# Optimization experiments

Hardware: AMD Instinct MI355X
Metric: run time of the kernel (lower is better)

Reference implementation:

```python
import jax, jax.numpy as jnp
import numpy as np

NUM_HEADS = 8
DIM = 384
KSIZE = 9  # res_kernel_size


def _moe_fc(x2d, gate_w, gate_b, w0, b0, w1, b1):
    # NaiveGate with top_k=1: softmax over a single top-1 logit == 1.0, so the
    # SparseDispatcher dispatch/exp/mul/log combine reduces exactly to selecting
    # the argmax expert's output per token.
    logits = x2d @ gate_w + gate_b                      # [T, 2]
    sel = jnp.argmax(logits, axis=-1)[:, None]          # [T, 1]
    y0 = x2d @ w0.T + b0
    y1 = x2d @ w1.T + b1
    return jnp.where(sel == 0, y0, y1)


def _forward(x, qkv_gate_w, qkv_gate_b, qkv_w0, qkv_w1,
             proj_gate_w, proj_gate_b, proj_w0, proj_b0, proj_w1, proj_b1,
             dconv_w):
    B, N, C = x.shape
    h, hd = NUM_HEADS, C // NUM_HEADS
    xt = x.reshape(-1, C)
    zero3 = jnp.zeros((3 * C,), x.dtype)  # qkv_bias=False
    qkv = _moe_fc(xt, qkv_gate_w, qkv_gate_b, qkv_w0, zero3, qkv_w1, zero3)
    qkv = qkv.reshape(B, N, 3, h, hd).transpose(2, 0, 3, 1, 4)  # [3,B,h,N,d]
    q, k, v = qkv[0], qkv[1], qkv[2]

    q = q / jnp.linalg.norm(q, axis=-1, keepdims=True)
    k = k / jnp.linalg.norm(k, axis=-1, keepdims=True)
    scale1 = jnp.mean(jnp.abs(q))
    scale2 = jnp.mean(jnp.abs(k))
    # straight-through binarization: fwd value = (x>0)*scale, grad flows via clamp(x,0,1)
    cq = jnp.clip(q, 0.0, 1.0)
    q = jax.lax.stop_gradient((q > 0).astype(q.dtype) * scale1 - cq) + cq
    ck = jnp.clip(k, 0.0, 1.0)
    k = jax.lax.stop_gradient((k > 0).astype(k.dtype) * scale2 - ck) + ck

    # depthwise residual conv over the token axis: v is [B, h, N, d], kernel (9,1)
    dconv_v = jax.lax.conv_general_dilated(
        v, dconv_w, window_strides=(1, 1), padding=[(KSIZE // 2, KSIZE // 2), (0, 0)],
        feature_group_count=h, dimension_numbers=("NCHW", "OIHW", "NCHW"))

    # linear-attention reorder: (K^T V) first -> O(N d^2)
    attn = jnp.einsum("bhnd,bhne->bhde", k, v)          # [B,h,d,d]
    out = 0.5 * v - (1.0 / jnp.pi) * jnp.einsum("bhnd,bhde->bhne", q, attn)
    out = out / jnp.linalg.norm(out, axis=-1, keepdims=True)
    out = out + dconv_v
    out = out.transpose(0, 2, 1, 3).reshape(B, N, C)

    out = _moe_fc(out.reshape(-1, C), proj_gate_w, proj_gate_b,
                  proj_w0, proj_b0, proj_w1, proj_b1)
    return out.reshape(B, N, C)


def setup_inputs() -> dict:
    key = jax.random.key(0)
    ks = jax.random.split(key, 12)
    B, N, C = 8, 4096, DIM
    s = 0.02
    return {
        "x": jax.random.normal(ks[0], (B, N, C), jnp.float32),
        "H": 64,
        "W": 64,
        "qkv_gate_w": jax.random.normal(ks[1], (C, 2), jnp.float32) * s,
        "qkv_gate_b": jnp.zeros((2,), jnp.float32),
        "qkv_w0": jax.random.normal(ks[2], (3 * C, C), jnp.float32) * s,
        "qkv_w1": jax.random.normal(ks[3], (3 * C, C), jnp.float32) * s,
        "proj_gate_w": jax.random.normal(ks[4], (C, 2), jnp.float32) * s,
        "proj_gate_b": jnp.zeros((2,), jnp.float32),
        "proj_w0": jax.random.normal(ks[5], (C, C), jnp.float32) * s,
        "proj_b0": jnp.zeros((C,), jnp.float32),
        "proj_w1": jax.random.normal(ks[6], (C, C), jnp.float32) * s,
        "proj_b1": jnp.zeros((C,), jnp.float32),
        "dconv_w": jax.random.normal(ks[7], (NUM_HEADS, 1, KSIZE, 1), jnp.float32) * s,
    }


def reference(x, H, W, qkv_gate_w, qkv_gate_b, qkv_w0, qkv_w1,
              proj_gate_w, proj_gate_b, proj_w0, proj_b0, proj_w1, proj_b1,
              dconv_w):
    # H, W are unused by the math (kept for signature fidelity)
    return _forward(x, qkv_gate_w, qkv_gate_b, qkv_w0, qkv_w1,
                    proj_gate_w, proj_gate_b, proj_w0, proj_b0, proj_w1, proj_b1,
                    dconv_w)
```

## Files before the change

kernel.cpp:

```cpp
#include <hip/hip_runtime.h>
#include <hip/hip_bf16.h>

#define BB 8
#define NN 4096
#define CC 384
#define HH 8
#define DD 48
#define TT (BB*NN)
#define CAP (TT + 128)
#define NQ ((size_t)BB*HH*NN*DD)
#define LISTCAP 32768

static_assert(CAP % 128 == 0, "cap");

typedef __attribute__((ext_vector_type(8))) short bf16x8;
typedef __attribute__((ext_vector_type(4))) float f32x4;

__device__ __forceinline__ float waveRedSum(float v){
  #pragma unroll
  for (int o = 32; o > 0; o >>= 1) v += __shfl_xor(v, o);
  return v;
}

__device__ __forceinline__ unsigned short f2bf(float f){
  unsigned u = __float_as_uint(f);
  u += 0x7FFFu + ((u >> 16) & 1u);
  return (unsigned short)(u >> 16);
}
__device__ __forceinline__ float bf2f(unsigned short h){
  return __uint_as_float(((unsigned)h) << 16);
}

__global__ void k_init(int* __restrict__ perm0, int* __restrict__ perm1, int* __restrict__ cur){
  int i = blockIdx.x * 256 + threadIdx.x;
  if (i < 8) cur[i] = 0;
  if (i < CAP){ perm0[i] = -1; perm1[i] = -1; }
}

__global__ void k_cvt_split(const float* __restrict__ src, unsigned short* __restrict__ hi,
                            unsigned short* __restrict__ lo, int n4){
  int i = blockIdx.x*256 + threadIdx.x;
  if (i >= n4) return;
  float4 v = ((const float4*)src)[i];
  float f[4] = {v.x, v.y, v.z, v.w};
  unsigned short h[4], l[4];
  #pragma unroll
  for (int j = 0; j < 4; j++){
    h[j] = f2bf(f[j]);
    l[j] = f2bf(f[j] - bf2f(h[j]));
  }
  uint2 hv, lv;
  hv.x = h[0] | ((unsigned)h[1] << 16); hv.y = h[2] | ((unsigned)h[3] << 16);
  lv.x = l[0] | ((unsigned)l[1] << 16); lv.y = l[2] | ((unsigned)l[3] << 16);
  ((uint2*)hi)[i] = hv;
  ((uint2*)lo)[i] = lv;
}

__global__ void k_gate_scatter(const float* __restrict__ X,
                               const float* __restrict__ gw, const float* __restrict__ gb,
                               int* __restrict__ perm, int* __restrict__ cur,
                               unsigned char* __restrict__ selb){
  const int lane = threadIdx.x & 63;
  const int wave = threadIdx.x >> 6;
  float gd[6];
  #pragma unroll
  for (int j = 0; j < 6; j++){
    int c = lane + 64*j;
    gd[j] = gw[c*2+1] - gw[c*2];
  }
  const float gbd = gb[1] - gb[0];
  const int tok0 = (blockIdx.x*4 + wave) * 32;
  unsigned mask = 0u;
  for (int i = 0; i < 32; i++){
    const float* xr = X + (size_t)(tok0 + i) * CC;
    float d = 0.f;
    #pragma unroll
    for (int j = 0; j < 6; j++) d = fmaf(xr[lane + 64*j], gd[j], d);
    d = waveRedSum(d);
    if (d + gbd > 0.f) mask |= (1u << i);
  }
  int n1 = __popc(mask), n0 = 32 - n1;
  int b0 = 0, b1 = 0;
  if (lane == 0){
    b0 = atomicAdd(cur + 0, n0);
    b1 = atomicAdd(cur + 1, n1);
  }
  b0 = __shfl(b0, 0); b1 = __shfl(b1, 0);
  if (lane < 32){
    int sel = (mask >> lane) & 1;
    unsigned below = mask & ((1u << lane) - 1u);
    int r1 = __popc(below);
    int r0 = lane - r1;
    int idx = sel ? (CAP - 1 - (b1 + r1)) : (b0 + r0);
    perm[idx] = tok0 + lane;
    selb[tok0 + lane] = (unsigned char)sel;
  }
}

__global__ void k_gate2(const float* __restrict__ gpart, const float* __restrict__ gb,
                        int* __restrict__ perm, int* __restrict__ cur){
  const int t = blockIdx.x*256 + threadIdx.x;
  const int lane = threadIdx.x & 63;
  const float gbd = gb[1] - gb[0];
  float4 a = ((const float4*)(gpart + (size_t)t*8))[0];
  float4 c = ((const float4*)(gpart + (size_t)t*8))[1];
  float d = ((a.x + a.y) + (a.z + a.w)) + ((c.x + c.y) + (c.z + c.w)) + gbd;
  bool sel = d > 0.f;
  unsigned long long m = __ballot(sel);
  int n1 = (int)__popcll(m);
  int b0 = 0, b1 = 0;
  if (lane == 0){
    b0 = atomicAdd(cur + 0, 64 - n1);
    b1 = atomicAdd(cur + 1, n1);
  }
  b0 = __shfl(b0, 0); b1 = __shfl(b1, 0);
  unsigned long long below = m & ((1ull << lane) - 1ull);
  int r1 = (int)__popcll(below);
  int r0 = lane - r1;
  int idx = sel ? (CAP - 1 - (b1 + r1)) : (b0 + r0);
  perm[idx] = t;
}

template<int NCOLS, int PASSES, bool IS_QKV>
__global__ __launch_bounds__(256, 2)
void k_gemm_mfma(const unsigned short* __restrict__ Ahi_g, const unsigned short* __restrict__ Alo_g,
                 const unsigned short* __restrict__ W0h, const unsigned short* __restrict__ W0l,
                 const unsigned short* __restrict__ W1h, const unsigned short* __restrict__ W1l,
                 const float* __restrict__ bias0, const float* __restrict__ bias1,
                 const int* __restrict__ perm, const int* __restrict__ cur,
                 unsigned short* __restrict__ oq, unsigned short* __restrict__ ok,
                 float* __restrict__ ov, float* __restrict__ oproj,
                 int* __restrict__ tlist, int* __restrict__ tcnt)
{
  constexpr int GDX = NCOLS / 128;
  constexpr int NWG = GDX * (CAP/128);
  constexpr int NB = (PASSES == 3) ? 2 : 1;
  __shared__ unsigned short As[NB][128*32];
  __shared__ unsigned short Bs[NB][128*32];
  __shared__ int permv[128];

  int orig = blockIdx.y * GDX + blockIdx.x;
  constexpr int qq = NWG >> 3, rr = NWG & 7;
  int xcd = orig & 7, slot = orig >> 3;
  int logical = (xcd < rr) ? (xcd*(qq+1) + slot) : (rr*(qq+1) + (xcd-rr)*qq + slot);
  const int bx = logical % GDX, by = logical / GDX;

  const int tid = threadIdx.x;
  const int m0 = by * 128, n0 = bx * 128;
  if (tid < 128) permv[tid] = perm[m0 + tid];
  __syncthreads();
  const int expert = (m0 > cur[0]) ? 1 : 0;
  const unsigned short* Wh = expert ? W1h : W0h;
  const unsigned short* Wl = expert ? W1l : W0l;

  const int c0 = tid, c1 = tid + 256;
  const int r0 = c0 >> 2, r1 = c1 >> 2;
  const int s0 = (((c0 & 3) ^ ((r0 >> 1) & 3))) * 8;
  const int s1 = (((c1 & 3) ^ ((r1 >> 1) & 3))) * 8;
  int t0 = permv[r0]; if (t0 < 0) t0 = 0;
  int t1 = permv[r1]; if (t1 < 0) t1 = 0;
  const unsigned short* a0h = Ahi_g + (size_t)t0*CC + s0;
  const unsigned short* a1h = Ahi_g + (size_t)t1*CC + s1;
  const unsigned short* b0h = Wh + (size_t)(n0 + r0)*CC + s0;
  const unsigned short* b1h = Wh + (size_t)(n0 + r1)*CC + s1;
  const unsigned short* a0l = nullptr; const unsigned short* a1l = nullptr;
  const unsigned short* b0l = nullptr; const unsigned short* b1l = nullptr;
  if constexpr (PASSES == 3){
    a0l = Alo_g + (size_t)t0*CC + s0;
    a1l = Alo_g + (size_t)t1*CC + s1;
    b0l = Wl + (size_t)(n0 + r0)*CC + s0;
    b1l = Wl + (size_t)(n0 + r1)*CC + s1;
  }
  const int d0 = c0*8, d1 = c1*8;

  const int lane = tid & 63;
  const int wv = tid >> 6, wr = wv >> 1, wc2 = wv & 1;
  const int lr = lane & 15, lg = lane >> 4;

  f32x4 acc[4][4];
  #pragma unroll
  for (int i = 0; i < 4; i++)
    #pragma unroll
    for (int j = 0; j < 4; j++) acc[i][j] = (f32x4){0.f, 0.f, 0.f, 0.f};

  int aoff[4], boff[4];
  #pragma unroll
  for (int f = 0; f < 4; f++){
    int ra = wr*64 + f*16 + lr;
    aoff[f] = ra*32 + ((lg ^ ((ra >> 1) & 3)) * 8);
    int rb = wc2*64 + f*16 + lr;
    boff[f] = rb*32 + ((lg ^ ((rb >> 1) & 3)) * 8);
  }

  #define GLD(gp, lp) __builtin_amdgcn_global_load_lds( \
      (const __attribute__((address_space(1))) void*)(gp), \
      (__attribute__((address_space(3))) void*)(lp), 16, 0, 0)

  for (int ko = 0; ko < CC; ko += 32){
    GLD(a0h + ko, &As[0][d0]);
    GLD(a1h + ko, &As[0][d1]);
    GLD(b0h + ko, &Bs[0][d0]);
    GLD(b1h + ko, &Bs[0][d1]);
    if constexpr (PASSES == 3){
      GLD(a0l + ko, &As[1][d0]);
      GLD(a1l + ko, &As[1][d1]);
      GLD(b0l + ko, &Bs[1][d0]);
      GLD(b1l + ko, &Bs[1][d1]);
    }
    __syncthreads();
    bf16x8 ah[4], bh[4], al[4], bl[4];
    #pragma unroll
    for (int f = 0; f < 4; f++){
      ah[f] = *(const bf16x8*)&As[0][aoff[f]];
      bh[f] = *(const bf16x8*)&Bs[0][boff[f]];
      if constexpr (PASSES == 3){
        al[f] = *(const bf16x8*)&As[1][aoff[f]];
        bl[f] = *(const bf16x8*)&Bs[1][boff[f]];
      }
    }
    #pragma unroll
    for (int mf = 0; mf < 4; mf++)
      #pragma unroll
      for (int nf = 0; nf < 4; nf++){
        acc[mf][nf] = __builtin_amdgcn_mfma_f32_16x16x32_bf16(ah[mf], bh[nf], acc[mf][nf], 0, 0, 0);
        if constexpr (PASSES == 3){
          acc[mf][nf] = __builtin_amdgcn_mfma_f32_16x16x32_bf16(al[mf], bh[nf], acc[mf][nf], 0, 0, 0);
          acc[mf][nf] = __builtin_amdgcn_mfma_f32_16x16x32_bf16(ah[mf], bl[nf], acc[mf][nf], 0, 0, 0);
        }
      }
    __syncthreads();
  }
  #undef GLD

  #pragma unroll
  for (int mf = 0; mf < 4; mf++){
    #pragma unroll
    for (int j = 0; j < 4; j++){
      const int rl = wr*64 + mf*16 + lg*4 + j;
      const int t = permv[rl];
      if (t < 0) continue;
      const int b = t >> 12, nn = t & 4095;
      #pragma unroll
      for (int nf = 0; nf < 4; nf++){
        const int col = n0 + wc2*64 + nf*16 + lr;
        const float val = acc[mf][nf][j];
        if constexpr (IS_QKV){
          const int which = col / CC;
          const int rem = col - which*CC;
          const int h = rem / DD;
          const int e = rem - h*DD;
          const size_t off = (((size_t)b*HH + h)*NN + nn)*DD + e;
          if (which == 0){
            oq[off] = f2bf(val);
            if (fabsf(val) < 2.5e-5f){
              int pq = atomicAdd(tcnt, 1);
              if (pq < LISTCAP) tlist[pq] = (int)off;
            }
          } else if (which == 1){
            ok[off] = f2bf(val);
            if (fabsf(val) < 2.5e-5f){
              int pq = atomicAdd(tcnt, 1);
              if (pq < LISTCAP) tlist[pq] = (int)(off + NQ);
            }
          } else {
            ov[off] = val;
          }
        } else {
          const float* bs = expert ? bias1 : bias0;
          oproj[(size_t)t*CC + col] = val + bs[col];
        }
      }
    }
  }
}

__global__ void k_topup_fix(unsigned short* __restrict__ qb, unsigned short* __restrict__ kb,
                            const int* __restrict__ list, const int* __restrict__ cnt,
                            const float* __restrict__ x,
                            const float* __restrict__ w0, const float* __restrict__ w1,
                            const unsigned char* __restrict__ selb){
  const int lane = threadIdx.x & 63;
  const int gw = (blockIdx.x*256 + threadIdx.x) >> 6;
  const int nwaves = gridDim.x * 4;
  int n = cnt[0]; if (n > LISTCAP) n = LISTCAP;
  for (int e = gw; e < n; e += nwaves){
    int idx = list[e];
    int isK = (idx >= (int)NQ);
    int li = isK ? idx - (int)NQ : idx;
    int d = li % DD; int rest = li / DD;
    int nn = rest & 4095; int bh = rest >> 12;
    int b = bh >> 3, h = bh & 7;
    int t = b*NN + nn;
    int col = (isK ? CC : 0) + h*DD + d;
    const float* w = selb[t] ? w1 : w0;
    const float* xr = x + (size_t)t*CC;
    const float* wr = w + (size_t)col*CC;
    float s = 0.f;
    #pragma unroll
    for (int j = 0; j < 6; j++) s = fmaf(xr[lane + 64*j], wr[lane + 64*j], s);
    s = waveRedSum(s);
    if (lane == 0) (isK ? kb : qb)[li] = f2bf(s);
  }
}

__global__ void k_scales(const unsigned short* __restrict__ qb, const unsigned short* __restrict__ kb,
                         float* __restrict__ part){
  __shared__ float sq[256], sk[256];
  const int row = blockIdx.x*256 + threadIdx.x;
  const uint4* qp = (const uint4*)(qb + (size_t)row*DD);
  const uint4* kp = (const uint4*)(kb + (size_t)row*DD);
  float qss = 0.f, qsa = 0.f, kss = 0.f, ksa = 0.f;
  #pragma unroll
  for (int j = 0; j < 6; j++){
    uint4 u = qp[j];
    unsigned w[4] = {u.x, u.y, u.z, u.w};
    #pragma unroll
    for (int q2 = 0; q2 < 4; q2++){
      float f0 = bf2f((unsigned short)(w[q2] & 0xFFFFu));
      float f1 = bf2f((unsigned short)(w[q2] >> 16));
      qss = fmaf(f0, f0, qss); qsa += fabsf(f0);
      qss = fmaf(f1, f1, qss); qsa += fabsf(f1);
    }
    uint4 v = kp[j];
    unsigned w2[4] = {v.x, v.y, v.z, v.w};
    #pragma unroll
    for (int q2 = 0; q2 < 4; q2++){
      float f0 = bf2f((unsigned short)(w2[q2] & 0xFFFFu));
      float f1 = bf2f((unsigned short)(w2[q2] >> 16));
      kss = fmaf(f0, f0, kss); ksa += fabsf(f0);
      kss = fmaf(f1, f1, kss); ksa += fabsf(f1);
    }
  }
  sq[threadIdx.x] = qsa / sqrtf(qss);
  sk[threadIdx.x] = ksa / sqrtf(kss);
  __syncthreads();
  for (int s = 128; s > 0; s >>= 1){
    if (threadIdx.x < s){ sq[threadIdx.x] += sq[threadIdx.x+s]; sk[threadIdx.x] += sk[threadIdx.x+s]; }
    __syncthreads();
  }
  if (threadIdx.x == 0){
    part[blockIdx.x*2+0] = sq[0];
    part[blockIdx.x*2+1] = sk[0];
  }
}

__global__ void k_scales_reduce(const float* __restrict__ part, float* __restrict__ scalesb){
  __shared__ float sq[256], sk[256];
  const int t = threadIdx.x;
  float aq = 0.f, ak = 0.f;
  for (int i = t; i < 1024; i += 256){ aq += part[2*i]; ak += part[2*i+1]; }
  sq[t] = aq; sk[t] = ak;
  __syncthreads();
  for (int s = 128; s > 0; s >>= 1){
    if (t < s){ sq[t] += sq[t+s]; sk[t] += sk[t+s]; }
    __syncthreads();
  }
  if (t == 0){
    scalesb[0] = sq[0] * (1.0f/12582912.0f);
    scalesb[1] = sk[0] * (1.0f/12582912.0f);
  }
}

__global__ void k_attn_partial(const unsigned short* __restrict__ kb, const float* __restrict__ vb,
                               float* __restrict__ part){
  __shared__ float ks[64][48];
  __shared__ float vs[64][48];
  const int bh = blockIdx.x, seg = blockIdx.y;
  const int tid = threadIdx.x;
  const int ti = tid >> 5;
  const int tj = (tid >> 2) & 7;
  const int sl = tid & 3;
  const int dd0 = ti*6, ee0 = tj*6;
  const unsigned short* kbase = kb + ((size_t)bh*NN + seg*512) * DD;
  const float* vbase = vb + ((size_t)bh*NN + seg*512) * DD;
  float acc[6][6] = {};
  for (int c = 0; c < 8; c++){
    __syncthreads();
    for (int f = tid*2; f < 3072; f += 512){
      unsigned kk2 = *(const unsigned*)(kbase + c*3072 + f);
      float2 vv2 = *(const float2*)(vbase + c*3072 + f);
      (&ks[0][0])[f]   = ((short)(unsigned short)(kk2 & 0xFFFFu) > 0) ? 1.f : 0.f;
      (&ks[0][0])[f+1] = ((short)(unsigned short)(kk2 >> 16) > 0) ? 1.f : 0.f;
      (&vs[0][0])[f]   = vv2.x;
      (&vs[0][0])[f+1] = vv2.y;
    }
    __syncthreads();
    for (int nl = sl*16; nl < sl*16 + 16; nl++){
      float kk[6], vv[6];
      #pragma unroll
      for (int i = 0; i < 6; i++){ kk[i] = ks[nl][dd0+i]; vv[i] = vs[nl][ee0+i]; }
      #pragma unroll
      for (int i = 0; i < 6; i++)
        #pragma unroll
        for (int j = 0; j < 6; j++)
          acc[i][j] = fmaf(kk[i], vv[j], acc[i][j]);
    }
  }
  float* p = part + ((size_t)seg*64 + bh) * (DD*DD);
  #pragma unroll
  for (int i = 0; i < 6; i++)
    #pragma unroll
    for (int j = 0; j < 6; j++){
      float a = acc[i][j];
      a += __shfl_xor(a, 1);
      a += __shfl_xor(a, 2);
      if (sl == 0) p[(dd0+i)*48 + (ee0+j)] = a;
    }
}

__global__ void k_attn_reduce(const float* __restrict__ part, const float* __restrict__ scalesb,
                              unsigned short* __restrict__ aTh, unsigned short* __restrict__ aTl){
  const int bh = blockIdx.x;
  const float s2 = scalesb[1];
  for (int f = threadIdx.x; f < 3072; f += 256){
    const int e = f >> 6, d = f & 63;
    float s = 0.f;
    if (d < 48){
      #pragma unroll
      for (int seg = 0; seg < 8; seg++) s += part[((size_t)seg*64 + bh)*2304 + d*48 + e];
      s *= s2;
    }
    unsigned short hi = f2bf(s);
    aTh[(size_t)bh*3072 + f] = hi;
    aTl[(size_t)bh*3072 + f] = f2bf(s - bf2f(hi));
  }
}

__global__ __launch_bounds__(256, 4)
void k_fused(const unsigned short* __restrict__ qb, const float* __restrict__ vb,
             const unsigned short* __restrict__ aTh, const unsigned short* __restrict__ aTl,
             const float* __restrict__ scalesb, const float* __restrict__ dw,
             const float* __restrict__ pgw,
             unsigned short* __restrict__ intermh, float* __restrict__ gpart){
  __shared__ unsigned short aT[2][48*72];
  __shared__ float S_lds[128*48];
  __shared__ float wc[16];
  const int chunk = blockIdx.x;
  const int bh = blockIdx.y;
  const int b = bh >> 3, h = bh & 7;
  const int tid = threadIdx.x;
  const int lane = tid & 63, w = tid >> 6;
  const int lr = lane & 15, lg = lane >> 4;

  for (int idx = tid; idx < 384; idx += 256){
    const int e = idx >> 3, sl = idx & 7;
    *(uint4*)&aT[0][e*72 + sl*8] = *(const uint4*)(aTh + (size_t)bh*3072 + e*64 + sl*8);
    *(uint4*)&aT[1][e*72 + sl*8] = *(const uint4*)(aTl + (size_t)bh*3072 + e*64 + sl*8);
  }
  if (tid < 9) wc[tid] = dw[h*9 + tid];
  __syncthreads();

  bf16x8 afr[2][2];
  #pragma unroll
  for (int m = 0; m < 2; m++){
    #pragma unroll
    for (int ks = 0; ks < 2; ks++){
      const int d0 = ks*32 + lg*8;
      bf16x8 a = (bf16x8){0,0,0,0,0,0,0,0};
      if (d0 < 48){
        const int tok = chunk*128 + (w*2+m)*16 + lr;
        uint4 raw = *(const uint4*)(qb + ((size_t)bh*NN + tok)*DD + d0);
        unsigned wd[4] = {raw.x, raw.y, raw.z, raw.w};
        #pragma unroll
        for (int i2 = 0; i2 < 8; i2++){
          unsigned short el = (unsigned short)((wd[i2 >> 1] >> ((i2 & 1)*16)) & 0xFFFFu);
          a[i2] = ((short)el > 0) ? (short)0x3F80 : (short)0;
        }
      }
      afr[m][ks] = a;
    }
  }
  f32x4 acc[2][3];
  #pragma unroll
  for (int m = 0; m < 2; m++)
    #pragma unroll
    for (int nf = 0; nf < 3; nf++) acc[m][nf] = (f32x4){0.f,0.f,0.f,0.f};
  #pragma unroll
  for (int nf = 0; nf < 3; nf++){
    bf16x8 bhv[2], blv[2];
    #pragma unroll
    for (int ks = 0; ks < 2; ks++){
      const int bo = (nf*16 + lr)*72 + ks*32 + lg*8;
      bhv[ks] = *(const bf16x8*)&aT[0][bo];
      blv[ks] = *(const bf16x8*)&aT[1][bo];
    }
    #pragma unroll
    for (int m = 0; m < 2; m++)
      #pragma unroll
      for (int ks = 0; ks < 2; ks++){
        acc[m][nf] = __builtin_amdgcn_mfma_f32_16x16x32_bf16(afr[m][ks], bhv[ks], acc[m][nf], 0, 0, 0);
        acc[m][nf] = __builtin_amdgcn_mfma_f32_16x16x32_bf16(afr[m][ks], blv[ks], acc[m][nf], 0, 0, 0);
      }
  }
  #pragma unroll
  for (int m = 0; m < 2; m++)
    #pragma unroll
    for (int nf = 0; nf < 3; nf++)
      #pragma unroll
      for (int j = 0; j < 4; j++)
        S_lds[((w*2+m)*16 + lg*4 + j)*48 + nf*16 + lr] = acc[m][nf][j];
  __syncthreads();

  const float coef = scalesb[0] * 0.31830988618379067f;
  const float gdh = (lane < 48) ? (pgw[(h*48+lane)*2+1] - pgw[(h*48+lane)*2]) : 0.f;
  const float* vrow = vb + (size_t)bh*NN*DD;
  const int n0 = chunk*128 + w*32;
  float ring[9];
  #pragma unroll
  for (int k2 = 0; k2 < 8; k2++){
    int nn2 = n0 - 4 + k2;
    ring[k2] = (nn2 >= 0 && nn2 < NN && lane < 48) ? vrow[(size_t)nn2*DD + lane] : 0.f;
  }
  for (int it = 0; it < 32; it++){
    const int n = n0 + it;
    const int nh = n + 4;
    ring[8] = (nh < NN && lane < 48) ? vrow[(size_t)nh*DD + lane] : 0.f;
    const float vv = ring[4];
    const float Sv = (lane < 48) ? S_lds[(w*32 + it)*48 + lane] : 0.f;
    float op = 0.5f*vv - coef*Sv;
    float ss = waveRedSum(op*op);
    float res = op / sqrtf(ss);
    float dc = 0.f;
    #pragma unroll
    for (int k2 = 0; k2 < 9; k2++) dc = fmaf(wc[k2], ring[k2], dc);
    float r = res + dc;
    if (lane < 48)
      intermh[((size_t)b*NN + n)*CC + h*DD + lane] = f2bf(r);
    float gp = waveRedSum(r*gdh);
    if (lane == 0) gpart[((size_t)b*NN + n)*8 + h] = gp;
    #pragma unroll
    for (int k2 = 0; k2 < 8; k2++) ring[k2] = ring[k2+1];
  }
}

extern "C" void kernel_launch(void* const* d_in, const int* in_sizes, int n_in,
                              void* d_out, int out_size, void* d_ws, size_t ws_size,
                              hipStream_t stream){
  const float* x    = (const float*)d_in[0];
  const float* qgw  = (const float*)d_in[3];
  const float* qgb  = (const float*)d_in[4];
  const float* qw0  = (const float*)d_in[5];
  const float* qw1  = (const float*)d_in[6];
  const float* pgw  = (const float*)d_in[7];
  const float* pgb  = (const float*)d_in[8];
  const float* pw0  = (const float*)d_in[9];
  const float* pb0  = (const float*)d_in[10];
  const float* pw1  = (const float*)d_in[11];
  const float* pb1  = (const float*)d_in[12];
  const float* dw   = (const float*)d_in[13];
  float* out = (float*)d_out;

  char* p = (char*)d_ws;
  auto alloc = [&](size_t bytes){ char* r = p; p += (bytes + 255) & ~(size_t)255; return r; };

  unsigned short* qbuf = (unsigned short*)alloc(2*NQ);
  unsigned short* kbuf = (unsigned short*)alloc(2*NQ);
  float* vbuf          = (float*)alloc(4*NQ);
  char* xreg           = alloc(4*NQ);
  unsigned short* Xhi  = (unsigned short*)xreg;
  unsigned short* Xlo  = Xhi + NQ;
  unsigned short* intermh = (unsigned short*)xreg;
  unsigned short* qw0h = (unsigned short*)alloc(2*1152*384);
  unsigned short* qw0l = (unsigned short*)alloc(2*1152*384);
  unsigned short* qw1h = (unsigned short*)alloc(2*1152*384);
  unsigned short* qw1l = (unsigned short*)alloc(2*1152*384);
  unsigned short* pw0h = (unsigned short*)alloc(2*384*384);
  unsigned short* pw0l = (unsigned short*)alloc(2*384*384);
  unsigned short* pw1h = (unsigned short*)alloc(2*384*384);
  unsigned short* pw1l = (unsigned short*)alloc(2*384*384);
  float* attn_part     = (float*)alloc(4*(size_t)8*64*2304);
  unsigned short* aTh  = (unsigned short*)alloc(2*(size_t)64*3072);
  unsigned short* aTl  = (unsigned short*)alloc(2*(size_t)64*3072);
  float* scale_part    = (float*)alloc(4*2048);
  float* scalesb       = (float*)alloc(64);
  float* gpart         = (float*)alloc(4*(size_t)TT*8);
  int* perm_qkv        = (int*)alloc(4*CAP);
  int* perm_proj       = (int*)alloc(4*CAP);
  int* cur             = (int*)alloc(64);
  int* list            = (int*)alloc(4*LISTCAP);
  unsigned char* selq  = (unsigned char*)alloc(TT);

  k_init<<<(CAP + 255)/256, 256, 0, stream>>>(perm_qkv, perm_proj, cur);

  k_cvt_split<<<(int)(NQ/4 + 255)/256, 256, 0, stream>>>(x, Xhi, Xlo, (int)(NQ/4));
  k_cvt_split<<<(1152*384/4 + 255)/256, 256, 0, stream>>>(qw0, qw0h, qw0l, 1152*384/4);
  k_cvt_split<<<(1152*384/4 + 255)/256, 256, 0, stream>>>(qw1, qw1h, qw1l, 1152*384/4);
  k_cvt_split<<<(384*384/4 + 255)/256, 256, 0, stream>>>(pw0, pw0h, pw0l, 384*384/4);
  k_cvt_split<<<(384*384/4 + 255)/256, 256, 0, stream>>>(pw1, pw1h, pw1l, 384*384/4);

  k_gate_scatter<<<256, 256, 0, stream>>>(x, qgw, qgb, perm_qkv, cur, selq);

  {
    dim3 g(9, CAP/128);
    k_gemm_mfma<1152, 3, true><<<g, 256, 0, stream>>>(
        Xhi, Xlo, qw0h, qw0l, qw1h, qw1l, nullptr, nullptr,
        perm_qkv, cur, qbuf, kbuf, vbuf, nullptr, list, cur + 4);
  }

  k_topup_fix<<<64, 256, 0, stream>>>(qbuf, kbuf, list, cur + 4, x, qw0, qw1, selq);

  k_scales<<<1024, 256, 0, stream>>>(qbuf, kbuf, scale_part);
  k_scales_reduce<<<1, 256, 0, stream>>>(scale_part, scalesb);

  {
    dim3 g(64, 8);
    k_attn_partial<<<g, 256, 0, stream>>>(kbuf, vbuf, attn_part);
  }
  k_attn_reduce<<<64, 256, 0, stream>>>(attn_part, scalesb, aTh, aTl);

  {
    dim3 g(32, 64);
    k_fused<<<g, 256, 0, stream>>>(qbuf, vbuf, aTh, aTl, scalesb, dw, pgw, intermh, gpart);
  }

  k_gate2<<<TT/256, 256, 0, stream>>>(gpart, pgb, perm_proj, cur + 2);

  {
    dim3 g(3, CAP/128);
    k_gemm_mfma<384, 1, false><<<g, 256, 0, stream>>>(
        intermh, nullptr, pw0h, pw0l, pw1h, pw1l, pb0, pb1,
        perm_proj, cur + 2, nullptr, nullptr, nullptr, out, nullptr, nullptr);
  }
}
```

Baseline: 378.5 us.

## Load GEMM operands directly from global and split fp32 activations on the fly

New measurement: 614.7 us. +62.4%, slower.

```diff
diff --git a/kernel.cpp b/kernel.cpp
--- a/kernel.cpp
+++ b/kernel.cpp
@@ -31,6 +31,22 @@
   return __uint_as_float(((unsigned)h) << 16);
 }
 
+__device__ __forceinline__ void split8(const float* __restrict__ p, bf16x8& hi, bf16x8& lo){
+  float4 r0 = *(const float4*)p;
+  float4 r1 = *(const float4*)(p + 4);
+  float f[8] = {r0.x, r0.y, r0.z, r0.w, r1.x, r1.y, r1.z, r1.w};
+  #pragma unroll
+  for (int i = 0; i < 8; i++){
+    unsigned u = __float_as_uint(f[i]);
+    unsigned r = u + 0x7FFFu + ((u >> 16) & 1u);
+    hi[i] = (short)(r >> 16);
+    float hf = __uint_as_float(r & 0xFFFF0000u);
+    float lf = f[i] - hf;
+    unsigned ul = __float_as_uint(lf);
+    lo[i] = (short)((ul + 0x7FFFu + ((ul >> 16) & 1u)) >> 16);
+  }
+}
+
 __global__ void k_init(int* __restrict__ perm0, int* __restrict__ perm1, int* __restrict__ cur){
   int i = blockIdx.x * 256 + threadIdx.x;
   if (i < 8) cur[i] = 0;
@@ -69,9 +85,9 @@
     gd[j] = gw[c*2+1] - gw[c*2];
   }
   const float gbd = gb[1] - gb[0];
-  const int tok0 = (blockIdx.x*4 + wave) * 32;
+  const int tok0 = (blockIdx.x*4 + wave) * 8;
   unsigned mask = 0u;
-  for (int i = 0; i < 32; i++){
+  for (int i = 0; i < 8; i++){
     const float* xr = X + (size_t)(tok0 + i) * CC;
     float d = 0.f;
     #pragma unroll
@@ -79,14 +95,14 @@
     d = waveRedSum(d);
     if (d + gbd > 0.f) mask |= (1u << i);
   }
-  int n1 = __popc(mask), n0 = 32 - n1;
+  int n1 = __popc(mask), n0 = 8 - n1;
   int b0 = 0, b1 = 0;
   if (lane == 0){
     b0 = atomicAdd(cur + 0, n0);
     b1 = atomicAdd(cur + 1, n1);
   }
   b0 = __shfl(b0, 0); b1 = __shfl(b1, 0);
-  if (lane < 32){
+  if (lane < 8){
     int sel = (mask >> lane) & 1;
     unsigned below = mask & ((1u << lane) - 1u);
     int r1 = __popc(below);
@@ -123,21 +139,17 @@
 
 template<int NCOLS, int PASSES, bool IS_QKV>
 __global__ __launch_bounds__(256, 2)
-void k_gemm_mfma(const unsigned short* __restrict__ Ahi_g, const unsigned short* __restrict__ Alo_g,
-                 const unsigned short* __restrict__ W0h, const unsigned short* __restrict__ W0l,
-                 const unsigned short* __restrict__ W1h, const unsigned short* __restrict__ W1l,
-                 const float* __restrict__ bias0, const float* __restrict__ bias1,
-                 const int* __restrict__ perm, const int* __restrict__ cur,
-                 unsigned short* __restrict__ oq, unsigned short* __restrict__ ok,
-                 float* __restrict__ ov, float* __restrict__ oproj,
-                 int* __restrict__ tlist, int* __restrict__ tcnt)
+void k_gemm_direct(const float* __restrict__ Af32, const unsigned short* __restrict__ Abf,
+                   const unsigned short* __restrict__ W0h, const unsigned short* __restrict__ W0l,
+                   const unsigned short* __restrict__ W1h, const unsigned short* __restrict__ W1l,
+                   const float* __restrict__ bias0, const float* __restrict__ bias1,
+                   const int* __restrict__ perm, const int* __restrict__ cur,
+                   unsigned short* __restrict__ oq, unsigned short* __restrict__ ok,
+                   float* __restrict__ ov, float* __restrict__ oproj,
+                   int* __restrict__ tlist, int* __restrict__ tcnt)
 {
   constexpr int GDX = NCOLS / 128;
   constexpr int NWG = GDX * (CAP/128);
-  constexpr int NB = (PASSES == 3) ? 2 : 1;
-  __shared__ unsigned short As[NB][128*32];
-  __shared__ unsigned short Bs[NB][128*32];
-  __shared__ int permv[128];
 
   int orig = blockIdx.y * GDX + blockIdx.x;
   constexpr int qq = NWG >> 3, rr = NWG & 7;
@@ -147,104 +159,78 @@
 
   const int tid = threadIdx.x;
   const int m0 = by * 128, n0 = bx * 128;
-  if (tid < 128) permv[tid] = perm[m0 + tid];
-  __syncthreads();
-  const int expert = (m0 > cur[0]) ? 1 : 0;
-  const unsigned short* Wh = expert ? W1h : W0h;
-  const unsigned short* Wl = expert ? W1l : W0l;
-
-  const int c0 = tid, c1 = tid + 256;
-  const int r0 = c0 >> 2, r1 = c1 >> 2;
-  const int s0 = (((c0 & 3) ^ ((r0 >> 1) & 3))) * 8;
-  const int s1 = (((c1 & 3) ^ ((r1 >> 1) & 3))) * 8;
-  int t0 = permv[r0]; if (t0 < 0) t0 = 0;
-  int t1 = permv[r1]; if (t1 < 0) t1 = 0;
-  const unsigned short* a0h = Ahi_g + (size_t)t0*CC + s0;
-  const unsigned short* a1h = Ahi_g + (size_t)t1*CC + s1;
-  const unsigned short* b0h = Wh + (size_t)(n0 + r0)*CC + s0;
-  const unsigned short* b1h = Wh + (size_t)(n0 + r1)*CC + s1;
-  const unsigned short* a0l = nullptr; const unsigned short* a1l = nullptr;
-  const unsigned short* b0l = nullptr; const unsigned short* b1l = nullptr;
-  if constexpr (PASSES == 3){
-    a0l = Alo_g + (size_t)t0*CC + s0;
-    a1l = Alo_g + (size_t)t1*CC + s1;
-    b0l = Wl + (size_t)(n0 + r0)*CC + s0;
-    b1l = Wl + (size_t)(n0 + r1)*CC + s1;
-  }
-  const int d0 = c0*8, d1 = c1*8;
-
   const int lane = tid & 63;
   const int wv = tid >> 6, wr = wv >> 1, wc2 = wv & 1;
   const int lr = lane & 15, lg = lane >> 4;
 
+  const int expert = (m0 > cur[0]) ? 1 : 0;
+  const unsigned short* __restrict__ Wh = expert ? W1h : W0h;
+  const unsigned short* __restrict__ Wl = expert ? W1l : W0l;
+
+  const float* ap32[4];
+  const unsigned short* ap16[4];
+  #pragma unroll
+  for (int f = 0; f < 4; f++){
+    int t = perm[m0 + wr*64 + f*16 + lr];
+    t = (t < 0) ? 0 : t;
+    if (IS_QKV) ap32[f] = Af32 + (size_t)t*CC + lg*8;
+    else        ap16[f] = Abf  + (size_t)t*CC + lg*8;
+  }
+  const unsigned short* bph[4];
+  const unsigned short* bpl[4];
+  #pragma unroll
+  for (int nf = 0; nf < 4; nf++){
+    const int col = n0 + wc2*64 + nf*16 + lr;
+    bph[nf] = Wh + (size_t)col*CC + lg*8;
+    if (PASSES == 3) bpl[nf] = Wl + (size_t)col*CC + lg*8;
+  }
+
   f32x4 acc[4][4];
   #pragma unroll
   for (int i = 0; i < 4; i++)
     #pragma unroll
     for (int j = 0; j < 4; j++) acc[i][j] = (f32x4){0.f, 0.f, 0.f, 0.f};
 
-  int aoff[4], boff[4];
-  #pragma unroll
-  for (int f = 0; f < 4; f++){
-    int ra = wr*64 + f*16 + lr;
-    aoff[f] = ra*32 + ((lg ^ ((ra >> 1) & 3)) * 8);
-    int rb = wc2*64 + f*16 + lr;
-    boff[f] = rb*32 + ((lg ^ ((rb >> 1) & 3)) * 8);
-  }
-
-  #define GLD(gp, lp) __builtin_amdgcn_global_load_lds( \
-      (const __attribute__((address_space(1))) void*)(gp), \
-      (__attribute__((address_space(3))) void*)(lp), 16, 0, 0)
-
   for (int ko = 0; ko < CC; ko += 32){
-    GLD(a0h + ko, &As[0][d0]);
-    GLD(a1h + ko, &As[0][d1]);
-    GLD(b0h + ko, &Bs[0][d0]);
-    GLD(b1h + ko, &Bs[0][d1]);
-    if constexpr (PASSES == 3){
-      GLD(a0l + ko, &As[1][d0]);
-      GLD(a1l + ko, &As[1][d1]);
-      GLD(b0l + ko, &Bs[1][d0]);
-      GLD(b1l + ko, &Bs[1][d1]);
-    }
-    __syncthreads();
-    bf16x8 ah[4], bh[4], al[4], bl[4];
+    bf16x8 ah[4], al[4], bh[4], bl[4];
     #pragma unroll
     for (int f = 0; f < 4; f++){
-      ah[f] = *(const bf16x8*)&As[0][aoff[f]];
-      bh[f] = *(const bf16x8*)&Bs[0][boff[f]];
-      if constexpr (PASSES == 3){
-        al[f] = *(const bf16x8*)&As[1][aoff[f]];
-        bl[f] = *(const bf16x8*)&Bs[1][boff[f]];
+      if (IS_QKV){
+        split8(ap32[f] + ko, ah[f], al[f]);
+      } else {
+        ah[f] = *(const bf16x8*)(ap16[f] + ko);
       }
+    }
+    #pragma unroll
+    for (int nf = 0; nf < 4; nf++){
+      bh[nf] = *(const bf16x8*)(bph[nf] + ko);
+      if (PASSES == 3) bl[nf] = *(const bf16x8*)(bpl[nf] + ko);
     }
     #pragma unroll
     for (int mf = 0; mf < 4; mf++)
       #pragma unroll
       for (int nf = 0; nf < 4; nf++){
         acc[mf][nf] = __builtin_amdgcn_mfma_f32_16x16x32_bf16(ah[mf], bh[nf], acc[mf][nf], 0, 0, 0);
-        if constexpr (PASSES == 3){
+        if (PASSES == 3){
           acc[mf][nf] = __builtin_amdgcn_mfma_f32_16x16x32_bf16(al[mf], bh[nf], acc[mf][nf], 0, 0, 0);
           acc[mf][nf] = __builtin_amdgcn_mfma_f32_16x16x32_bf16(ah[mf], bl[nf], acc[mf][nf], 0, 0, 0);
         }
       }
-    __syncthreads();
-  }
-  #undef GLD
+  }
 
   #pragma unroll
   for (int mf = 0; mf < 4; mf++){
     #pragma unroll
     for (int j = 0; j < 4; j++){
       const int rl = wr*64 + mf*16 + lg*4 + j;
-      const int t = permv[rl];
+      const int t = perm[m0 + rl];
       if (t < 0) continue;
       const int b = t >> 12, nn = t & 4095;
       #pragma unroll
       for (int nf = 0; nf < 4; nf++){
         const int col = n0 + wc2*64 + nf*16 + lr;
         const float val = acc[mf][nf][j];
-        if constexpr (IS_QKV){
+        if (IS_QKV){
           const int which = col / CC;
           const int rem = col - which*CC;
           const int h = rem / DD;
@@ -556,10 +542,7 @@
   unsigned short* qbuf = (unsigned short*)alloc(2*NQ);
   unsigned short* kbuf = (unsigned short*)alloc(2*NQ);
   float* vbuf          = (float*)alloc(4*NQ);
-  char* xreg           = alloc(4*NQ);
-  unsigned short* Xhi  = (unsigned short*)xreg;
-  unsigned short* Xlo  = Xhi + NQ;
-  unsigned short* intermh = (unsigned short*)xreg;
+  unsigned short* intermh = (unsigned short*)alloc(2*NQ);
   unsigned short* qw0h = (unsigned short*)alloc(2*1152*384);
   unsigned short* qw0l = (unsigned short*)alloc(2*1152*384);
   unsigned short* qw1h = (unsigned short*)alloc(2*1152*384);
@@ -582,18 +565,17 @@
 
   k_init<<<(CAP + 255)/256, 256, 0, stream>>>(perm_qkv, perm_proj, cur);
 
-  k_cvt_split<<<(int)(NQ/4 + 255)/256, 256, 0, stream>>>(x, Xhi, Xlo, (int)(NQ/4));
   k_cvt_split<<<(1152*384/4 + 255)/256, 256, 0, stream>>>(qw0, qw0h, qw0l, 1152*384/4);
   k_cvt_split<<<(1152*384/4 + 255)/256, 256, 0, stream>>>(qw1, qw1h, qw1l, 1152*384/4);
   k_cvt_split<<<(384*384/4 + 255)/256, 256, 0, stream>>>(pw0, pw0h, pw0l, 384*384/4);
   k_cvt_split<<<(384*384/4 + 255)/256, 256, 0, stream>>>(pw1, pw1h, pw1l, 384*384/4);
 
-  k_gate_scatter<<<256, 256, 0, stream>>>(x, qgw, qgb, perm_qkv, cur, selq);
+  k_gate_scatter<<<1024, 256, 0, stream>>>(x, qgw, qgb, perm_qkv, cur, selq);
 
   {
     dim3 g(9, CAP/128);
-    k_gemm_mfma<1152, 3, true><<<g, 256, 0, stream>>>(
-        Xhi, Xlo, qw0h, qw0l, qw1h, qw1l, nullptr, nullptr,
+    k_gemm_direct<1152, 3, true><<<g, 256, 0, stream>>>(
+        x, nullptr, qw0h, qw0l, qw1h, qw1l, nullptr, nullptr,
         perm_qkv, cur, qbuf, kbuf, vbuf, nullptr, list, cur + 4);
   }
 
@@ -617,8 +599,8 @@
 
   {
     dim3 g(3, CAP/128);
-    k_gemm_mfma<384, 1, false><<<g, 256, 0, stream>>>(
-        intermh, nullptr, pw0h, pw0l, pw1h, pw1l, pb0, pb1,
+    k_gemm_direct<384, 1, false><<<g, 256, 0, stream>>>(
+        nullptr, intermh, pw0h, nullptr, pw1h, nullptr, pb0, pb1,
         perm_proj, cur + 2, nullptr, nullptr, nullptr, out, nullptr, nullptr);
   }
 }
```

## Double-buffer LDS tiles in MoE GEMM to overlap loads with MFMA

Applied to the files above, without the earlier changes.

New measurement: 393.8 us. 4.0% more time.

```diff
diff --git a/kernel.cpp b/kernel.cpp
--- a/kernel.cpp
+++ b/kernel.cpp
@@ -135,8 +135,8 @@
   constexpr int GDX = NCOLS / 128;
   constexpr int NWG = GDX * (CAP/128);
   constexpr int NB = (PASSES == 3) ? 2 : 1;
-  __shared__ unsigned short As[NB][128*32];
-  __shared__ unsigned short Bs[NB][128*32];
+  __shared__ unsigned short As[2][NB][128*32];
+  __shared__ unsigned short Bs[2][NB][128*32];
   __shared__ int permv[128];
 
   int orig = blockIdx.y * GDX + blockIdx.x;
@@ -196,26 +196,42 @@
       (const __attribute__((address_space(1))) void*)(gp), \
       (__attribute__((address_space(3))) void*)(lp), 16, 0, 0)
 
+  #define STAGE(bi, KO) do { \
+    GLD(a0h + (KO), &As[bi][0][d0]); \
+    GLD(a1h + (KO), &As[bi][0][d1]); \
+    GLD(b0h + (KO), &Bs[bi][0][d0]); \
+    GLD(b1h + (KO), &Bs[bi][0][d1]); \
+    if constexpr (PASSES == 3){ \
+      GLD(a0l + (KO), &As[bi][1][d0]); \
+      GLD(a1l + (KO), &As[bi][1][d1]); \
+      GLD(b0l + (KO), &Bs[bi][1][d0]); \
+      GLD(b1l + (KO), &Bs[bi][1][d1]); \
+    } \
+  } while(0)
+
+  STAGE(0, 0);
   for (int ko = 0; ko < CC; ko += 32){
-    GLD(a0h + ko, &As[0][d0]);
-    GLD(a1h + ko, &As[0][d1]);
-    GLD(b0h + ko, &Bs[0][d0]);
-    GLD(b1h + ko, &Bs[0][d1]);
-    if constexpr (PASSES == 3){
-      GLD(a0l + ko, &As[1][d0]);
-      GLD(a1l + ko, &As[1][d1]);
-      GLD(b0l + ko, &Bs[1][d0]);
-      GLD(b1l + ko, &Bs[1][d1]);
-    }
-    __syncthreads();
+    const int cb = (ko >> 5) & 1;
+    const bool have_next = (ko + 32 < CC);
+    if (have_next) STAGE(cb ^ 1, ko + 32);
+
+    if (have_next){
+      if constexpr (PASSES == 3) asm volatile("s_waitcnt vmcnt(8)" ::: "memory");
+      else                       asm volatile("s_waitcnt vmcnt(4)" ::: "memory");
+    } else {
+      asm volatile("s_waitcnt vmcnt(0)" ::: "memory");
+    }
+    __builtin_amdgcn_sched_barrier(0);
+    __builtin_amdgcn_s_barrier();
+
     bf16x8 ah[4], bh[4], al[4], bl[4];
     #pragma unroll
     for (int f = 0; f < 4; f++){
-      ah[f] = *(const bf16x8*)&As[0][aoff[f]];
-      bh[f] = *(const bf16x8*)&Bs[0][boff[f]];
+      ah[f] = *(const bf16x8*)&As[cb][0][aoff[f]];
+      bh[f] = *(const bf16x8*)&Bs[cb][0][boff[f]];
       if constexpr (PASSES == 3){
-        al[f] = *(const bf16x8*)&As[1][aoff[f]];
-        bl[f] = *(const bf16x8*)&Bs[1][boff[f]];
+        al[f] = *(const bf16x8*)&As[cb][1][aoff[f]];
+        bl[f] = *(const bf16x8*)&Bs[cb][1][boff[f]];
       }
     }
     #pragma unroll
@@ -228,8 +244,9 @@
           acc[mf][nf] = __builtin_amdgcn_mfma_f32_16x16x32_bf16(ah[mf], bl[nf], acc[mf][nf], 0, 0, 0);
         }
       }
-    __syncthreads();
-  }
+    __builtin_amdgcn_s_barrier();
+  }
+  #undef STAGE
   #undef GLD
 
   #pragma unroll
```
